# Performance work log

Measured on AMD Instinct MI355X. Metric: run time of the kernel, lower is better.

Reference implementation:

```python
import jax, jax.numpy as jnp
import numpy as np

# Mamba2 hyperparams (from config['block'][0])
D_MODEL = 512
D_STATE = 64
D_CONV = 4
EXPAND = 2
HEADDIM = 64
D_INNER = EXPAND * D_MODEL          # 1024
NHEADS = D_INNER // HEADDIM         # 16
CONV_DIM = D_INNER + 2 * D_STATE    # 1152 (x, B, C share the depthwise conv)
D_IN_PROJ = 2 * D_INNER + 2 * D_STATE + NHEADS  # z | xBC | dt
EPS = 1e-5
BATCH, SEQLEN = 2, 4096


def setup_inputs() -> dict:
    key = jax.random.key(0)
    ks = jax.random.split(key, 10)
    x = jax.random.normal(ks[0], (BATCH, SEQLEN, D_MODEL), dtype=jnp.float32)
    W_in = jax.random.normal(ks[1], (D_MODEL, D_IN_PROJ), dtype=jnp.float32) * 0.02
    conv_w = jax.random.normal(ks[2], (CONV_DIM, 1, D_CONV), dtype=jnp.float32) * 0.2
    conv_b = jax.random.normal(ks[3], (CONV_DIM,), dtype=jnp.float32) * 0.02
    dt_bias = jax.random.uniform(ks[4], (NHEADS,), minval=-4.0, maxval=-1.0, dtype=jnp.float32)
    A_log = jnp.log(jax.random.uniform(ks[5], (NHEADS,), minval=1.0, maxval=16.0, dtype=jnp.float32))
    D = jax.random.normal(ks[6], (NHEADS,), dtype=jnp.float32) * 0.5 + 1.0
    norm_weight = jnp.ones((D_INNER,), dtype=jnp.float32)
    W_out = jax.random.normal(ks[7], (D_INNER, D_MODEL), dtype=jnp.float32) * 0.02
    return {"x": x, "W_in": W_in, "conv_w": conv_w, "conv_b": conv_b,
            "dt_bias": dt_bias, "A_log": A_log, "D": D,
            "norm_weight": norm_weight, "W_out": W_out}


def _mamba2_forward(x, W_in, conv_w, conv_b, dt_bias, A_log, D, norm_weight, W_out):
    b, l, _ = x.shape
    zxbcdt = x @ W_in                                      # (b, l, D_IN_PROJ)
    z = zxbcdt[..., :D_INNER]                              # gate branch
    xBC = zxbcdt[..., D_INNER:D_INNER + CONV_DIM]
    dt = zxbcdt[..., D_INNER + CONV_DIM:]                  # (b, l, h)

    # depthwise causal conv1d over sequence, then SiLU
    xBC_ncw = jnp.transpose(xBC, (0, 2, 1))                # (b, c, l)
    xBC_ncw = jax.lax.conv_general_dilated(
        xBC_ncw, conv_w, window_strides=(1,), padding=[(D_CONV - 1, 0)],
        dimension_numbers=("NCW", "OIW", "NCW"), feature_group_count=CONV_DIM)
    xBC_ncw = xBC_ncw + conv_b[None, :, None]
    xBC = jax.nn.silu(jnp.transpose(xBC_ncw, (0, 2, 1)))   # (b, l, c)

    x_ssm = xBC[..., :D_INNER].reshape(b, l, NHEADS, HEADDIM)  # (b,l,h,p)
    B = xBC[..., D_INNER:D_INNER + D_STATE]                    # (b,l,n)
    C = xBC[..., D_INNER + D_STATE:]                           # (b,l,n)

    dt = jax.nn.softplus(dt + dt_bias)                     # (b,l,h)
    A = -jnp.exp(A_log)                                    # (h,)
    dA = jnp.exp(dt * A)                                   # (b,l,h) discrete decay

    # selective scan: state s has shape (b, h, p, n)
    def step(s, inp):
        dA_t, dt_t, x_t, B_t, C_t = inp                    # (b,h),(b,h),(b,h,p),(b,n),(b,n)
        dBx = (dt_t[..., None] * x_t)[..., None] * B_t[:, None, None, :]
        s = s * dA_t[..., None, None] + dBx
        y_t = jnp.einsum("bhpn,bn->bhp", s, C_t)
        return s, y_t

    s0 = jnp.zeros((b, NHEADS, HEADDIM, D_STATE), dtype=x.dtype)
    xs = (jnp.moveaxis(dA, 1, 0), jnp.moveaxis(dt, 1, 0),
          jnp.moveaxis(x_ssm, 1, 0), jnp.moveaxis(B, 1, 0), jnp.moveaxis(C, 1, 0))
    _, ys = jax.lax.scan(step, s0, xs)                     # ys: (l,b,h,p)
    y = jnp.moveaxis(ys, 0, 1)                             # (b,l,h,p)

    y = y + D[None, None, :, None] * x_ssm                 # skip term
    y = y.reshape(b, l, D_INNER)

    # gated RMSNorm (norm after gating, mamba2 default)
    y = y * jax.nn.silu(z)
    var = jnp.mean(jnp.square(y), axis=-1, keepdims=True)
    y = y * jax.lax.rsqrt(var + EPS) * norm_weight

    return y @ W_out                                       # (b, l, d_model)


def reference(x, W_in, conv_w, conv_b, dt_bias, A_log, D, norm_weight, W_out):
    return _mamba2_forward(x, W_in, conv_w, conv_b, dt_bias, A_log, D, norm_weight, W_out)
```

## Files before the change

kernel.cpp:

```cpp
#include <hip/hip_runtime.h>
#include <hip/hip_bf16.h>

#define BATCH   2
#define SEQ     4096
#define DMODEL  512
#define DINNER  1024
#define DSTATE  64
#define NHEADS  16
#define HEADDIM 64
#define CONVDIM 1152
#define NPROJ   2192
#define NPROJ_PAD 2304
#define MROWS   (BATCH*SEQ)
#define QCH     64
#define NCHUNK  (SEQ/QCH)

typedef short bf16x8 __attribute__((ext_vector_type(8)));
typedef float f32x4  __attribute__((ext_vector_type(4)));
using bf16 = __hip_bfloat16;
typedef unsigned short ushort_t;
typedef unsigned int   uint_t;

__device__ __forceinline__ float sigmoidf_(float x) { return 1.f / (1.f + __expf(-x)); }
__device__ __forceinline__ float bf2f(ushort_t u) { return __uint_as_float((uint_t)u << 16); }
__device__ __forceinline__ ushort_t f2bfu(float f) {
    bf16 h = __float2bfloat16(f);
    return *(ushort_t*)&h;
}
__device__ __forceinline__ void bf8_to_f(const ushort_t* __restrict__ p, float* __restrict__ f) {
    uint4 u = *(const uint4*)p;
    f[0] = __uint_as_float((u.x & 0xFFFFu) << 16);
    f[1] = __uint_as_float(u.x & 0xFFFF0000u);
    f[2] = __uint_as_float((u.y & 0xFFFFu) << 16);
    f[3] = __uint_as_float(u.y & 0xFFFF0000u);
    f[4] = __uint_as_float((u.z & 0xFFFFu) << 16);
    f[5] = __uint_as_float(u.z & 0xFFFF0000u);
    f[6] = __uint_as_float((u.w & 0xFFFFu) << 16);
    f[7] = __uint_as_float(u.w & 0xFFFF0000u);
}
__device__ __forceinline__ uint4 f8_to_bf(const float* __restrict__ f) {
    union { ushort_t s[8]; uint4 u; } r;
#pragma unroll
    for (int i = 0; i < 8; i++) r.s[i] = f2bfu(f[i]);
    return r.u;
}

__device__ __forceinline__ void gload_lds16(const ushort_t* g, ushort_t* l)
{
    __builtin_amdgcn_global_load_lds(
        (const __attribute__((address_space(1))) void*)g,
        (__attribute__((address_space(3)))       void*)l,
        16, 0, 0);
}

__global__ void cast_f32_bf16_k(const float* __restrict__ in, ushort_t* __restrict__ out, int n8)
{
    int i = blockIdx.x * 256 + threadIdx.x;
    if (i >= n8) return;
    float f[8];
    *(float4*)(f + 0) = ((const float4*)in)[i * 2 + 0];
    *(float4*)(f + 4) = ((const float4*)in)[i * 2 + 1];
    ((uint4*)out)[i] = f8_to_bf(f);
}

__global__ void transpose_f32_bf16_k(const float* __restrict__ in, ushort_t* __restrict__ out,
                                     int R, int C, int Cpad, const float* __restrict__ sv)
{
    __shared__ __align__(16) ushort_t tile[32][33];
    int c0 = blockIdx.x * 32, r0 = blockIdx.y * 32;
    int tx = threadIdx.x, ty = threadIdx.y;
#pragma unroll
    for (int i = 0; i < 32; i += 8) {
        int r = r0 + ty + i, c = c0 + tx;
        float v = (r < R && c < C) ? in[(size_t)r * C + c] : 0.f;
        if (sv && r < R) v *= sv[r];
        tile[ty + i][tx] = f2bfu(v);
    }
    __syncthreads();
#pragma unroll
    for (int i = 0; i < 32; i += 8) {
        int orow = c0 + ty + i, ocol = r0 + tx;
        if (orow < Cpad && ocol < R) out[(size_t)orow * R + ocol] = tile[tx][ty + i];
    }
}

__global__ void bcconv_k(const ushort_t* __restrict__ xpbc, const float* __restrict__ cw,
                         const float* __restrict__ cb, ushort_t* __restrict__ bcc)
{
    int idx = blockIdx.x * 256 + threadIdx.x;
    int row = idx >> 4, c8 = (idx & 15) * 8;
    int l = row & (SEQ - 1);
    float acc[8];
#pragma unroll
    for (int i = 0; i < 8; i++) acc[i] = cb[1024 + c8 + i];
#pragma unroll
    for (int j = 0; j < 4; j++) {
        int ll = l - 3 + j;
        if (ll >= 0) {
            float v[8];
            bf8_to_f(xpbc + (size_t)(row - 3 + j) * 128 + c8, v);
#pragma unroll
            for (int i = 0; i < 8; i++) acc[i] += cw[(1024 + c8 + i) * 4 + j] * v[i];
        }
    }
#pragma unroll
    for (int i = 0; i < 8; i++) { float v = acc[i]; acc[i] = v * sigmoidf_(v); }
    *(uint4*)(bcc + (size_t)row * 128 + c8) = f8_to_bf(acc);
}

__global__ __launch_bounds__(256, 4)
void xconv_k(const ushort_t* __restrict__ xpre, const float* __restrict__ cw,
             const float* __restrict__ cb, ushort_t* __restrict__ xs)
{
    const int c8 = (threadIdx.x & 127) * 8;
    const int rh = threadIdx.x >> 7;
    const int b  = blockIdx.y;
    const int l0 = blockIdx.x * 32 + rh * 16;
    float w[4][8], cbv[8];
#pragma unroll
    for (int i = 0; i < 8; i++) {
        cbv[i] = cb[c8 + i];
        float4 wv = *(const float4*)(cw + (size_t)(c8 + i) * 4);
        w[0][i] = wv.x; w[1][i] = wv.y; w[2][i] = wv.z; w[3][i] = wv.w;
    }
    float win[3][8];
#pragma unroll
    for (int j = 0; j < 3; j++) {
        int ll = l0 - 3 + j;
        if (ll >= 0) bf8_to_f(xpre + ((size_t)b * SEQ + ll) * 1024 + c8, win[j]);
        else {
#pragma unroll
            for (int i = 0; i < 8; i++) win[j][i] = 0.f;
        }
    }
#pragma unroll 4
    for (int r = 0; r < 16; r++) {
        int l = l0 + r;
        float cur[8], o[8];
        bf8_to_f(xpre + ((size_t)b * SEQ + l) * 1024 + c8, cur);
#pragma unroll
        for (int i = 0; i < 8; i++) {
            float a = cbv[i] + w[0][i] * win[0][i] + w[1][i] * win[1][i]
                             + w[2][i] * win[2][i] + w[3][i] * cur[i];
            o[i] = a * sigmoidf_(a);
        }
        *(uint4*)(xs + ((size_t)b * SEQ + l) * 1024 + c8) = f8_to_bf(o);
#pragma unroll
        for (int i = 0; i < 8; i++) { win[0][i] = win[1][i]; win[1][i] = win[2][i]; win[2][i] = cur[i]; }
    }
}

template<int MODE>
__global__ __launch_bounds__(256, MODE == 1 ? 4 : 3)
void gemm_k(const ushort_t* __restrict__ A, const ushort_t* __restrict__ Bt,
            ushort_t* __restrict__ zbuf, ushort_t* __restrict__ xpx,
            ushort_t* __restrict__ xpbc, float* __restrict__ dtv,
            float* __restrict__ dalog, const float* __restrict__ dt_b,
            const float* __restrict__ A_log, float* __restrict__ outf,
            int M, int N, int K)
{
    constexpr int TN = (MODE == 1) ? 64 : 128;
    constexpr int NJ = TN / 32;
    constexpr int SC = 132;
    constexpr int SMEM_ELTS = (MODE == 1) ? (128 * 64 + TN * 64) : (128 * SC);
    __shared__ __align__(16) ushort_t smem[SMEM_ELTS];
    ushort_t* As = smem;
    ushort_t* Bs = smem + 128 * 64;
    ushort_t* Cs = smem;

    const int tid  = threadIdx.x;
    const int wave = tid >> 6, lane = tid & 63;
    const int quad = lane >> 4, l16 = lane & 15;
    const int wm = (wave >> 1) * 64, wn = (wave & 1) * (TN / 2);

    const int GX = gridDim.x;
    int lin = blockIdx.y * GX + blockIdx.x;
    const int cpx = (GX * gridDim.y) >> 3;
    lin = (lin & 7) * cpx + (lin >> 3);
    const int m0 = (lin / GX) * 128, n0 = (lin % GX) * TN;

    const int srow = lane >> 3;
    const int scol = (lane & 7) * 8;
    const ushort_t* ag = A  + (size_t)(m0 + wave * 32       + srow) * K + scol;
    const ushort_t* bg = Bt + (size_t)(n0 + wave * (TN / 4) + srow) * K + scol;
    ushort_t* al = As + wave * 32 * 64;
    ushort_t* bl = Bs + wave * (TN / 4) * 64;

    f32x4 acc[4][NJ];
#pragma unroll
    for (int i = 0; i < 4; i++)
#pragma unroll
        for (int j = 0; j < NJ; j++) acc[i][j] = (f32x4){0.f, 0.f, 0.f, 0.f};
    float ssq4[4] = {0.f, 0.f, 0.f, 0.f};

    for (int k0 = 0; k0 < K; k0 += 64) {
        __syncthreads();
#pragma unroll
        for (int j = 0; j < 4; j++)
            gload_lds16(ag + (size_t)(j * 8) * K + k0, al + j * 8 * 64);
#pragma unroll
        for (int j = 0; j < NJ; j++)
            gload_lds16(bg + (size_t)(j * 8) * K + k0, bl + j * 8 * 64);
        __syncthreads();
#pragma unroll
        for (int kk = 0; kk < 64; kk += 32) {
            bf16x8 af[4], bfr[NJ];
#pragma unroll
            for (int i = 0; i < 4; i++)
                af[i] = *(const bf16x8*)(&As[(wm + i * 16 + l16) * 64 + kk + quad * 8]);
#pragma unroll
            for (int j = 0; j < NJ; j++)
                bfr[j] = *(const bf16x8*)(&Bs[(wn + j * 16 + l16) * 64 + kk + quad * 8]);
#pragma unroll
            for (int i = 0; i < 4; i++)
#pragma unroll
                for (int j = 0; j < NJ; j++)
                    acc[i][j] = __builtin_amdgcn_mfma_f32_16x16x32_bf16(af[i], bfr[j], acc[i][j], 0, 0, 0);
            if (MODE == 1 && (wave & 1) == 0) {
#pragma unroll
                for (int i = 0; i < 4; i++)
#pragma unroll
                    for (int e = 0; e < 8; e++) {
                        float f = bf2f((ushort_t)af[i][e]);
                        ssq4[i] += f * f;
                    }
            }
        }
    }
    if (MODE == 1) {
        __syncthreads();
        float* smemf = (float*)smem;
        if ((wave & 1) == 0) {
#pragma unroll
            for (int i = 0; i < 4; i++) {
                float s = ssq4[i];
                s += __shfl_xor(s, 16, 64);
                s += __shfl_xor(s, 32, 64);
                if (quad == 0) smemf[wm + i * 16 + l16] = s;
            }
        }
        __syncthreads();
#pragma unroll
        for (int i = 0; i < 4; i++)
#pragma unroll
            for (int j = 0; j < NJ; j++) {
                int col  = n0 + wn + j * 16 + l16;
                int rowl = wm + i * 16 + quad * 4;
#pragma unroll
                for (int r = 0; r < 4; r++) {
                    float sc = rsqrtf(smemf[rowl + r] * (1.f / DINNER) + 1e-5f);
                    outf[(size_t)(m0 + rowl + r) * N + col] = acc[i][j][r] * sc;
                }
            }
    } else if (n0 == 2176) {
#pragma unroll
        for (int i = 0; i < 4; i++)
#pragma unroll
            for (int j = 0; j < NJ; j++) {
                int col = n0 + wn + j * 16 + l16;
                int rowb = m0 + wm + i * 16 + quad * 4;
                if (col < N) {
                    int hh = col - 2176;
#pragma unroll
                    for (int r = 0; r < 4; r++) {
                        float v = acc[i][j][r];
                        size_t g = (size_t)hh * MROWS + (rowb + r);
                        float raw = v + dt_b[hh];
                        float sp  = (raw > 20.f) ? raw : log1pf(__expf(raw));
                        dtv  [g] = sp;
                        dalog[g] = -__expf(A_log[hh]) * sp;
                    }
                }
            }
    } else {
        __syncthreads();
#pragma unroll
        for (int i = 0; i < 4; i++)
#pragma unroll
            for (int j = 0; j < NJ; j++)
#pragma unroll
                for (int r = 0; r < 4; r++)
                    Cs[(wm + i * 16 + quad * 4 + r) * SC + wn + j * 16 + l16] = f2bfu(acc[i][j][r]);
        __syncthreads();
        ushort_t* dst; int ld, coff;
        if (n0 < 1024)      { dst = zbuf; ld = 1024; coff = n0; }
        else if (n0 < 2048) { dst = xpx;  ld = 1024; coff = n0 - 1024; }
        else                { dst = xpbc; ld = 128;  coff = 0; }
#pragma unroll
        for (int jj = 0; jj < 8; jj++) {
            int idx = jj * 256 + tid;
            int row = idx >> 4, cq = (idx & 15) * 8;
            uint4 v = *(const uint4*)&Cs[row * SC + cq];
            *(uint4*)&dst[(size_t)(m0 + row) * ld + coff + cq] = v;
        }
    }
}

__global__ __launch_bounds__(256, 3)
void chunk_state_k(const ushort_t* __restrict__ xs, const ushort_t* __restrict__ bcc,
                   const float* __restrict__ dtv, const float* __restrict__ dalog,
                   ushort_t* __restrict__ statesT, float* __restrict__ cdecay)
{
    const int c = blockIdx.x, h = blockIdx.y, b = blockIdx.z;
    __shared__ __align__(16) ushort_t xsT[64 * 72];
    __shared__ __align__(16) ushort_t BwT[64 * 72];
    __shared__ float wc[64];
    const int tid = threadIdx.x;
    const int ts = tid >> 2, q4 = (tid & 3) * 16;
    const int l = c * QCH + ts;
    if (tid < 64) {
        size_t gl = (size_t)h * MROWS + (size_t)b * SEQ + c * QCH + tid;
        float v = dalog[gl];
#pragma unroll
        for (int off = 1; off < 64; off <<= 1) {
            float u = __shfl_up(v, off, 64);
            if (tid >= off) v += u;
        }
        float tot = __shfl(v, 63, 64);
        wc[tid] = __expf(tot - v) * dtv[gl];
        if (tid == 63) cdecay[(c * BATCH + b) * NHEADS + h] = __expf(tot);
    }
    {
        const int ch0 = h * HEADDIM + q4;
        const ushort_t* rp = xs + ((size_t)b * SEQ + l) * 1024 + ch0;
        union { uint4 u; ushort_t s[8]; } u0, u1;
        u0.u = *(const uint4*)rp; u1.u = *(const uint4*)(rp + 8);
#pragma unroll
        for (int i = 0; i < 8; i++) {
            xsT[(q4 + i) * 72 + ts]     = u0.s[i];
            xsT[(q4 + 8 + i) * 72 + ts] = u1.s[i];
        }
    }
    __syncthreads();
    {
        float bv[16];
        const ushort_t* rp = bcc + ((size_t)b * SEQ + l) * 128;
        bf8_to_f(rp + q4, bv); bf8_to_f(rp + q4 + 8, bv + 8);
        const float wt = wc[ts];
#pragma unroll
        for (int i = 0; i < 16; i++) BwT[(q4 + i) * 72 + ts] = f2bfu(bv[i] * wt);
    }
    __syncthreads();
    const int wave = tid >> 6, lane = tid & 63;
    const int quad = lane >> 4, l16 = lane & 15;
    f32x4 acc[4];
#pragma unroll
    for (int j = 0; j < 4; j++) acc[j] = (f32x4){0.f, 0.f, 0.f, 0.f};
#pragma unroll
    for (int kk = 0; kk < 64; kk += 32) {
        bf16x8 af = *(const bf16x8*)(&xsT[(wave * 16 + l16) * 72 + kk + quad * 8]);
#pragma unroll
        for (int j = 0; j < 4; j++) {
            bf16x8 bf_ = *(const bf16x8*)(&BwT[(j * 16 + l16) * 72 + kk + quad * 8]);
            acc[j] = __builtin_amdgcn_mfma_f32_16x16x32_bf16(af, bf_, acc[j], 0, 0, 0);
        }
    }
    ushort_t* base = statesT + ((size_t)(c * BATCH + b) * NHEADS + h) * (HEADDIM * DSTATE);
#pragma unroll
    for (int j = 0; j < 4; j++)
#pragma unroll
        for (int r = 0; r < 4; r++)
            base[(wave * 16 + quad * 4 + r) * 64 + j * 16 + l16] = f2bfu(acc[j][r]);
}

__global__ void scan_combine_k(ushort_t* __restrict__ states, const float* __restrict__ cdecay)
{
    const int blk = blockIdx.x;
    const int eighth = blk & 7;
    const int h = (blk >> 3) & 15;
    const int b = blk >> 7;
    const int tid = threadIdx.x;
    __shared__ float dec[64];
    if (tid < 64) dec[tid] = cdecay[(tid * BATCH + b) * NHEADS + h];
    __syncthreads();
    const size_t cstride = (size_t)BATCH * NHEADS * HEADDIM * DSTATE;
    ushort_t* base = states + ((size_t)b * NHEADS + h) * (HEADDIM * DSTATE) + eighth * 512 + tid * 4;
    float sx = 0.f, sy = 0.f, sz = 0.f, sw = 0.f;
    uint2 pre[4];
#pragma unroll
    for (int j = 0; j < 4; j++) pre[j] = *(const uint2*)(base + j * cstride);
    for (int c = 0; c < NCHUNK; c++) {
        uint2 Sc = pre[c & 3];
        if (c + 4 < NCHUNK) pre[c & 3] = *(const uint2*)(base + (size_t)(c + 4) * cstride);
        float d = dec[c];
        uint2 o;
        o.x = (uint_t)f2bfu(sx) | ((uint_t)f2bfu(sy) << 16);
        o.y = (uint_t)f2bfu(sz) | ((uint_t)f2bfu(sw) << 16);
        *(uint2*)(base + (size_t)c * cstride) = o;
        sx = d * sx + __uint_as_float((Sc.x & 0xFFFFu) << 16);
        sy = d * sy + __uint_as_float(Sc.x & 0xFFFF0000u);
        sz = d * sz + __uint_as_float((Sc.y & 0xFFFFu) << 16);
        sw = d * sw + __uint_as_float(Sc.y & 0xFFFF0000u);
    }
}

__global__ __launch_bounds__(256, 3)
void chunk_y_k(const ushort_t* __restrict__ xs, const ushort_t* __restrict__ bcc,
               ushort_t* zio,
               const float* __restrict__ dtv, const float* __restrict__ dalog,
               const ushort_t* __restrict__ statesT, const float* __restrict__ Dp)
{
    const int c = blockIdx.x, h = blockIdx.y, b = blockIdx.z;
    __shared__ __align__(16) ushort_t CLb [64 * 72];
    __shared__ __align__(16) ushort_t BLb [64 * 72];
    __shared__ __align__(16) ushort_t xsT [64 * 72];
    __shared__ __align__(16) ushort_t attL[64 * 72];
    __shared__ float cum[64], wdt[64];
    const int tid = threadIdx.x;
    const int ts = tid >> 2, q4 = (tid & 3) * 16;
    const int l = c * QCH + ts;
    const float Dh = Dp[h];
    {
        const int ch0 = h * HEADDIM + q4;
        const ushort_t* rp = xs + ((size_t)b * SEQ + l) * 1024 + ch0;
        union { uint4 u; ushort_t s[8]; } u0, u1;
        u0.u = *(const uint4*)rp; u1.u = *(const uint4*)(rp + 8);
#pragma unroll
        for (int i = 0; i < 8; i++) {
            xsT[(q4 + i) * 72 + ts]     = u0.s[i];
            xsT[(q4 + 8 + i) * 72 + ts] = u1.s[i];
        }
    }
    {
        const ushort_t* rp = bcc + ((size_t)b * SEQ + l) * 128;
        *(uint4*)&BLb[ts * 72 + q4]     = *(const uint4*)(rp + q4);
        *(uint4*)&BLb[ts * 72 + q4 + 8] = *(const uint4*)(rp + q4 + 8);
        *(uint4*)&CLb[ts * 72 + q4]     = *(const uint4*)(rp + 64 + q4);
        *(uint4*)&CLb[ts * 72 + q4 + 8] = *(const uint4*)(rp + 64 + q4 + 8);
    }
    if (tid < 64) {
        size_t gl = (size_t)h * MROWS + (size_t)b * SEQ + c * QCH + tid;
        float v = dalog[gl];
#pragma unroll
        for (int off = 1; off < 64; off <<= 1) {
            float u = __shfl_up(v, off, 64);
            if (tid >= off) v += u;
        }
        cum[tid] = v;
        wdt[tid] = dtv[gl];
    }
    __syncthreads();
    const int wave = tid >> 6, lane = tid & 63;
    const int quad = lane >> 4, l16 = lane & 15;
    {
        f32x4 sacc[4];
#pragma unroll
        for (int j = 0; j < 4; j++) sacc[j] = (f32x4){0.f, 0.f, 0.f, 0.f};
#pragma unroll
        for (int kk = 0; kk < 64; kk += 32) {
            bf16x8 af = *(const bf16x8*)(&CLb[(wave * 16 + l16) * 72 + kk + quad * 8]);
#pragma unroll
            for (int j = 0; j < 4; j++) {
                bf16x8 bf_ = *(const bf16x8*)(&BLb[(j * 16 + l16) * 72 + kk + quad * 8]);
                sacc[j] = __builtin_amdgcn_mfma_f32_16x16x32_bf16(af, bf_, sacc[j], 0, 0, 0);
            }
        }
#pragma unroll
        for (int r = 0; r < 4; r++) {
            const int t = wave * 16 + quad * 4 + r;
            const float ct = cum[t];
#pragma unroll
            for (int j = 0; j < 4; j++) {
                const int s = j * 16 + l16;
                float a = (s <= t) ? sacc[j][r] * __expf(ct - cum[s]) * wdt[s] : 0.f;
                attL[t * 72 + s] = f2bfu(a);
            }
        }
    }
    __syncthreads();
    {
        f32x4 accY[4], accI[4];
#pragma unroll
        for (int j = 0; j < 4; j++) { accY[j] = (f32x4){0.f, 0.f, 0.f, 0.f}; accI[j] = (f32x4){0.f, 0.f, 0.f, 0.f}; }
        const ushort_t* spg = statesT + ((size_t)(c * BATCH + b) * NHEADS + h) * (HEADDIM * DSTATE);
#pragma unroll
        for (int kk = 0; kk < 64; kk += 32) {
            bf16x8 a2 = *(const bf16x8*)(&attL[(wave * 16 + l16) * 72 + kk + quad * 8]);
            bf16x8 a3 = *(const bf16x8*)(&CLb [(wave * 16 + l16) * 72 + kk + quad * 8]);
#pragma unroll
            for (int j = 0; j < 4; j++) {
                bf16x8 b2 = *(const bf16x8*)(&xsT[(j * 16 + l16) * 72 + kk + quad * 8]);
                accY[j] = __builtin_amdgcn_mfma_f32_16x16x32_bf16(a2, b2, accY[j], 0, 0, 0);
                bf16x8 b3 = *(const bf16x8*)(spg + (j * 16 + l16) * 64 + kk + quad * 8);
                accI[j] = __builtin_amdgcn_mfma_f32_16x16x32_bf16(a3, b3, accI[j], 0, 0, 0);
            }
        }
#pragma unroll
        for (int r = 0; r < 4; r++) {
            const int t = wave * 16 + quad * 4 + r;
            const float et = __expf(cum[t]);
#pragma unroll
            for (int j = 0; j < 4; j++) {
                const int p = j * 16 + l16;
                float xv = bf2f(xsT[p * 72 + t]);
                float y = accY[j][r] + et * accI[j][r] + Dh * xv;
                BLb[t * 72 + p] = f2bfu(y);
            }
        }
    }
    __syncthreads();
    {
        ushort_t* zrow = zio + ((size_t)b * SEQ + l) * DINNER + h * HEADDIM + q4;
        float zv[16], yv[16], o[16];
        bf8_to_f(zrow, zv); bf8_to_f(zrow + 8, zv + 8);
        bf8_to_f(&BLb[ts * 72 + q4], yv); bf8_to_f(&BLb[ts * 72 + q4 + 8], yv + 8);
#pragma unroll
        for (int j = 0; j < 16; j++) {
            float z = zv[j];
            o[j] = yv[j] * z * sigmoidf_(z);
        }
        *(uint4*)(zrow)     = f8_to_bf(o);
        *(uint4*)(zrow + 8) = f8_to_bf(o + 8);
    }
}

extern "C" void kernel_launch(void* const* d_in, const int* in_sizes, int n_in,
                              void* d_out, int out_size, void* d_ws, size_t ws_size,
                              hipStream_t stream)
{
    const float* x      = (const float*)d_in[0];
    const float* W_in   = (const float*)d_in[1];
    const float* conv_w = (const float*)d_in[2];
    const float* conv_b = (const float*)d_in[3];
    const float* dt_b   = (const float*)d_in[4];
    const float* A_log  = (const float*)d_in[5];
    const float* Dp     = (const float*)d_in[6];
    const float* nw     = (const float*)d_in[7];
    const float* W_out  = (const float*)d_in[8];
    float* out = (float*)d_out;

    char* w = (char*)d_ws;
    ushort_t* zbuf    = (ushort_t*)(w);
    ushort_t* xs      = (ushort_t*)(w + 16777216);
    ushort_t* xpre    = (ushort_t*)(w + 33554432);
    ushort_t* statesT = (ushort_t*)(w + 33554432);
    ushort_t* WoutT   = (ushort_t*)(w + 33554432);
    char* dscr = (char*)d_out;
    ushort_t* xpbc  = (ushort_t*)(dscr);
    float*    dtv   = (float*)(dscr + 2097152);
    float*    dalog = (float*)(dscr + 2621440);
    float*    cdec  = (float*)(dscr + 3145728);
    ushort_t* WinT  = (ushort_t*)(dscr + 4194304);
    ushort_t* bcc   = (ushort_t*)(dscr + 4194304);
    ushort_t* xb    = (ushort_t*)(dscr + 8388608);

    cast_f32_bf16_k<<<(MROWS * DMODEL / 8 + 255) / 256, 256, 0, stream>>>(x, xb, MROWS * DMODEL / 8);
    transpose_f32_bf16_k<<<dim3(NPROJ_PAD / 32, DMODEL / 32), dim3(32, 8), 0, stream>>>(W_in, WinT, DMODEL, NPROJ, NPROJ_PAD, nullptr);
    gemm_k<0><<<dim3(NPROJ_PAD / 128, MROWS / 128), 256, 0, stream>>>(
        xb, WinT, zbuf, xpre, xpbc, dtv, dalog, dt_b, A_log, nullptr,
        MROWS, NPROJ, DMODEL);
    bcconv_k<<<MROWS * 16 / 256, 256, 0, stream>>>(xpbc, conv_w, conv_b, bcc);
    xconv_k<<<dim3(SEQ / 32, BATCH), 256, 0, stream>>>(xpre, conv_w, conv_b, xs);
    chunk_state_k<<<dim3(NCHUNK, NHEADS, BATCH), 256, 0, stream>>>(
        xs, bcc, dtv, dalog, statesT, cdec);
    scan_combine_k<<<BATCH * NHEADS * 8, 128, 0, stream>>>(statesT, cdec);
    chunk_y_k<<<dim3(NCHUNK, NHEADS, BATCH), 256, 0, stream>>>(
        xs, bcc, zbuf, dtv, dalog, statesT, Dp);
    transpose_f32_bf16_k<<<dim3(DMODEL / 32, DINNER / 32), dim3(32, 8), 0, stream>>>(W_out, WoutT, DINNER, DMODEL, DMODEL, nw);
    gemm_k<1><<<dim3(DMODEL / 64, MROWS / 128), 256, 0, stream>>>(
        zbuf, WoutT, nullptr, nullptr, nullptr, nullptr, nullptr, nullptr,
        nullptr, out, MROWS, DMODEL, DINNER);
}
```

Baseline: 221.6 us.

## Merge prep and conv launches; XOR-swizzle transposed LDS tiles in chunk kernels

Combines the x cast and both weight transposes into one prep kernel, and the B/C conv and x conv into one conv kernel. This cuts the launch count by three. WoutT is moved into the output scratch region so it can be built at the start instead of after chunk_y. The transposed xsT/BwT stores and reads in chunk_state and chunk_y now use an XOR swizzle on the column index to reduce LDS bank conflicts during the column-wise writes. The swizzle must match on every read site; a missed index would corrupt results.

```diff
diff --git a/kernel.cpp b/kernel.cpp
--- a/kernel.cpp
+++ b/kernel.cpp
@@ -53,22 +53,35 @@
         16, 0, 0);
 }
 
-__global__ void cast_f32_bf16_k(const float* __restrict__ in, ushort_t* __restrict__ out, int n8)
-{
-    int i = blockIdx.x * 256 + threadIdx.x;
-    if (i >= n8) return;
-    float f[8];
-    *(float4*)(f + 0) = ((const float4*)in)[i * 2 + 0];
-    *(float4*)(f + 4) = ((const float4*)in)[i * 2 + 1];
-    ((uint4*)out)[i] = f8_to_bf(f);
-}
-
-__global__ void transpose_f32_bf16_k(const float* __restrict__ in, ushort_t* __restrict__ out,
-                                     int R, int C, int Cpad, const float* __restrict__ sv)
+__global__ __launch_bounds__(256, 4)
+void prep_k(const float* __restrict__ x, ushort_t* __restrict__ xb,
+            const float* __restrict__ W_in, ushort_t* __restrict__ WinT,
+            const float* __restrict__ W_out, ushort_t* __restrict__ WoutT,
+            const float* __restrict__ nw)
 {
     __shared__ __align__(16) ushort_t tile[32][33];
-    int c0 = blockIdx.x * 32, r0 = blockIdx.y * 32;
-    int tx = threadIdx.x, ty = threadIdx.y;
+    const int bid = blockIdx.x, tid = threadIdx.x;
+    if (bid < 2048) {
+        int i = bid * 256 + tid;
+        float f[8];
+        *(float4*)(f + 0) = ((const float4*)x)[i * 2 + 0];
+        *(float4*)(f + 4) = ((const float4*)x)[i * 2 + 1];
+        ((uint4*)xb)[i] = f8_to_bf(f);
+        return;
+    }
+    const int tx = tid & 31, ty = tid >> 5;
+    const float* in; ushort_t* out; int R, C, Cpad; const float* sv;
+    int bx, by;
+    if (bid < 3200) {
+        int b2 = bid - 2048;
+        bx = b2 % (NPROJ_PAD / 32); by = b2 / (NPROJ_PAD / 32);
+        in = W_in; out = WinT; R = DMODEL; C = NPROJ; Cpad = NPROJ_PAD; sv = nullptr;
+    } else {
+        int b3 = bid - 3200;
+        bx = b3 % (DMODEL / 32); by = b3 / (DMODEL / 32);
+        in = W_out; out = WoutT; R = DINNER; C = DMODEL; Cpad = DMODEL; sv = nw;
+    }
+    int c0 = bx * 32, r0 = by * 32;
 #pragma unroll
     for (int i = 0; i < 32; i += 8) {
         int r = r0 + ty + i, c = c0 + tx;
@@ -84,38 +97,39 @@
     }
 }
 
-__global__ void bcconv_k(const ushort_t* __restrict__ xpbc, const float* __restrict__ cw,
-                         const float* __restrict__ cb, ushort_t* __restrict__ bcc)
-{
-    int idx = blockIdx.x * 256 + threadIdx.x;
-    int row = idx >> 4, c8 = (idx & 15) * 8;
-    int l = row & (SEQ - 1);
-    float acc[8];
-#pragma unroll
-    for (int i = 0; i < 8; i++) acc[i] = cb[1024 + c8 + i];
-#pragma unroll
-    for (int j = 0; j < 4; j++) {
-        int ll = l - 3 + j;
-        if (ll >= 0) {
-            float v[8];
-            bf8_to_f(xpbc + (size_t)(row - 3 + j) * 128 + c8, v);
-#pragma unroll
-            for (int i = 0; i < 8; i++) acc[i] += cw[(1024 + c8 + i) * 4 + j] * v[i];
-        }
-    }
-#pragma unroll
-    for (int i = 0; i < 8; i++) { float v = acc[i]; acc[i] = v * sigmoidf_(v); }
-    *(uint4*)(bcc + (size_t)row * 128 + c8) = f8_to_bf(acc);
-}
-
 __global__ __launch_bounds__(256, 4)
-void xconv_k(const ushort_t* __restrict__ xpre, const float* __restrict__ cw,
-             const float* __restrict__ cb, ushort_t* __restrict__ xs)
-{
-    const int c8 = (threadIdx.x & 127) * 8;
-    const int rh = threadIdx.x >> 7;
-    const int b  = blockIdx.y;
-    const int l0 = blockIdx.x * 32 + rh * 16;
+void conv_k(const ushort_t* __restrict__ xpbc, const ushort_t* __restrict__ xpre,
+            const float* __restrict__ cw, const float* __restrict__ cb,
+            ushort_t* __restrict__ bcc, ushort_t* __restrict__ xs)
+{
+    const int bid = blockIdx.x, tid = threadIdx.x;
+    if (bid < 512) {
+        int idx = bid * 256 + tid;
+        int row = idx >> 4, c8 = (idx & 15) * 8;
+        int l = row & (SEQ - 1);
+        float acc[8];
+#pragma unroll
+        for (int i = 0; i < 8; i++) acc[i] = cb[1024 + c8 + i];
+#pragma unroll
+        for (int j = 0; j < 4; j++) {
+            int ll = l - 3 + j;
+            if (ll >= 0) {
+                float v[8];
+                bf8_to_f(xpbc + (size_t)(row - 3 + j) * 128 + c8, v);
+#pragma unroll
+                for (int i = 0; i < 8; i++) acc[i] += cw[(1024 + c8 + i) * 4 + j] * v[i];
+            }
+        }
+#pragma unroll
+        for (int i = 0; i < 8; i++) { float v = acc[i]; acc[i] = v * sigmoidf_(v); }
+        *(uint4*)(bcc + (size_t)row * 128 + c8) = f8_to_bf(acc);
+        return;
+    }
+    const int b2 = bid - 512;
+    const int gx = b2 & 127, b = b2 >> 7;
+    const int c8 = (tid & 127) * 8;
+    const int rh = tid >> 7;
+    const int l0 = gx * 32 + rh * 16;
     float w[4][8], cbv[8];
 #pragma unroll
     for (int i = 0; i < 8; i++) {
@@ -308,6 +322,7 @@
     const int tid = threadIdx.x;
     const int ts = tid >> 2, q4 = (tid & 3) * 16;
     const int l = c * QCH + ts;
+    const int tswz = ts ^ ((tid & 3) << 3);
     if (tid < 64) {
         size_t gl = (size_t)h * MROWS + (size_t)b * SEQ + c * QCH + tid;
         float v = dalog[gl];
@@ -327,8 +342,8 @@
         u0.u = *(const uint4*)rp; u1.u = *(const uint4*)(rp + 8);
 #pragma unroll
         for (int i = 0; i < 8; i++) {
-            xsT[(q4 + i) * 72 + ts]     = u0.s[i];
-            xsT[(q4 + 8 + i) * 72 + ts] = u1.s[i];
+            xsT[(q4 + i) * 72 + tswz]     = u0.s[i];
+            xsT[(q4 + 8 + i) * 72 + tswz] = u1.s[i];
         }
     }
     __syncthreads();
@@ -338,7 +353,7 @@
         bf8_to_f(rp + q4, bv); bf8_to_f(rp + q4 + 8, bv + 8);
         const float wt = wc[ts];
 #pragma unroll
-        for (int i = 0; i < 16; i++) BwT[(q4 + i) * 72 + ts] = f2bfu(bv[i] * wt);
+        for (int i = 0; i < 16; i++) BwT[(q4 + i) * 72 + tswz] = f2bfu(bv[i] * wt);
     }
     __syncthreads();
     const int wave = tid >> 6, lane = tid & 63;
@@ -348,10 +363,10 @@
     for (int j = 0; j < 4; j++) acc[j] = (f32x4){0.f, 0.f, 0.f, 0.f};
 #pragma unroll
     for (int kk = 0; kk < 64; kk += 32) {
-        bf16x8 af = *(const bf16x8*)(&xsT[(wave * 16 + l16) * 72 + kk + quad * 8]);
+        bf16x8 af = *(const bf16x8*)(&xsT[(wave * 16 + l16) * 72 + ((kk + quad * 8) ^ ((wave & 3) << 3))]);
 #pragma unroll
         for (int j = 0; j < 4; j++) {
-            bf16x8 bf_ = *(const bf16x8*)(&BwT[(j * 16 + l16) * 72 + kk + quad * 8]);
+            bf16x8 bf_ = *(const bf16x8*)(&BwT[(j * 16 + l16) * 72 + ((kk + quad * 8) ^ ((j & 3) << 3))]);
             acc[j] = __builtin_amdgcn_mfma_f32_16x16x32_bf16(af, bf_, acc[j], 0, 0, 0);
         }
     }
@@ -409,6 +424,7 @@
     const int tid = threadIdx.x;
     const int ts = tid >> 2, q4 = (tid & 3) * 16;
     const int l = c * QCH + ts;
+    const int tswz = ts ^ ((tid & 3) << 3);
     const float Dh = Dp[h];
     {
         const int ch0 = h * HEADDIM + q4;
@@ -417,8 +433,8 @@
         u0.u = *(const uint4*)rp; u1.u = *(const uint4*)(rp + 8);
 #pragma unroll
         for (int i = 0; i < 8; i++) {
-            xsT[(q4 + i) * 72 + ts]     = u0.s[i];
-            xsT[(q4 + 8 + i) * 72 + ts] = u1.s[i];
+            xsT[(q4 + i) * 72 + tswz]     = u0.s[i];
+            xsT[(q4 + 8 + i) * 72 + tswz] = u1.s[i];
         }
     }
     {
@@ -479,7 +495,7 @@
             bf16x8 a3 = *(const bf16x8*)(&CLb [(wave * 16 + l16) * 72 + kk + quad * 8]);
 #pragma unroll
             for (int j = 0; j < 4; j++) {
-                bf16x8 b2 = *(const bf16x8*)(&xsT[(j * 16 + l16) * 72 + kk + quad * 8]);
+                bf16x8 b2 = *(const bf16x8*)(&xsT[(j * 16 + l16) * 72 + ((kk + quad * 8) ^ ((j & 3) << 3))]);
                 accY[j] = __builtin_amdgcn_mfma_f32_16x16x32_bf16(a2, b2, accY[j], 0, 0, 0);
                 bf16x8 b3 = *(const bf16x8*)(spg + (j * 16 + l16) * 64 + kk + quad * 8);
                 accI[j] = __builtin_amdgcn_mfma_f32_16x16x32_bf16(a3, b3, accI[j], 0, 0, 0);
@@ -492,7 +508,7 @@
 #pragma unroll
             for (int j = 0; j < 4; j++) {
                 const int p = j * 16 + l16;
-                float xv = bf2f(xsT[p * 72 + t]);
+                float xv = bf2f(xsT[p * 72 + (t ^ ((j & 3) << 3))]);
                 float y = accY[j][r] + et * accI[j][r] + Dh * xv;
                 BLb[t * 72 + p] = f2bfu(y);
             }
@@ -534,7 +550,6 @@
     ushort_t* xs      = (ushort_t*)(w + 16777216);
     ushort_t* xpre    = (ushort_t*)(w + 33554432);
     ushort_t* statesT = (ushort_t*)(w + 33554432);
-    ushort_t* WoutT   = (ushort_t*)(w + 33554432);
     char* dscr = (char*)d_out;
     ushort_t* xpbc  = (ushort_t*)(dscr);
     float*    dtv   = (float*)(dscr + 2097152);
@@ -542,21 +557,20 @@
     float*    cdec  = (float*)(dscr + 3145728);
     ushort_t* WinT  = (ushort_t*)(dscr + 4194304);
     ushort_t* bcc   = (ushort_t*)(dscr + 4194304);
+    ushort_t* WoutT = (ushort_t*)(dscr + 6815744);
     ushort_t* xb    = (ushort_t*)(dscr + 8388608);
 
-    cast_f32_bf16_k<<<(MROWS * DMODEL / 8 + 255) / 256, 256, 0, stream>>>(x, xb, MROWS * DMODEL / 8);
-    transpose_f32_bf16_k<<<dim3(NPROJ_PAD / 32, DMODEL / 32), dim3(32, 8), 0, stream>>>(W_in, WinT, DMODEL, NPROJ, NPROJ_PAD, nullptr);
+    prep_k<<<2048 + (NPROJ_PAD / 32) * (DMODEL / 32) + (DMODEL / 32) * (DINNER / 32), 256, 0, stream>>>(
+        x, xb, W_in, WinT, W_out, WoutT, nw);
     gemm_k<0><<<dim3(NPROJ_PAD / 128, MROWS / 128), 256, 0, stream>>>(
         xb, WinT, zbuf, xpre, xpbc, dtv, dalog, dt_b, A_log, nullptr,
         MROWS, NPROJ, DMODEL);
-    bcconv_k<<<MROWS * 16 / 256, 256, 0, stream>>>(xpbc, conv_w, conv_b, bcc);
-    xconv_k<<<dim3(SEQ / 32, BATCH), 256, 0, stream>>>(xpre, conv_w, conv_b, xs);
+    conv_k<<<512 + 256, 256, 0, stream>>>(xpbc, xpre, conv_w, conv_b, bcc, xs);
     chunk_state_k<<<dim3(NCHUNK, NHEADS, BATCH), 256, 0, stream>>>(
         xs, bcc, dtv, dalog, statesT, cdec);
     scan_combine_k<<<BATCH * NHEADS * 8, 128, 0, stream>>>(statesT, cdec);
     chunk_y_k<<<dim3(NCHUNK, NHEADS, BATCH), 256, 0, stream>>>(
         xs, bcc, zbuf, dtv, dalog, statesT, Dp);
-    transpose_f32_bf16_k<<<dim3(DMODEL / 32, DINNER / 32), dim3(32, 8), 0, stream>>>(W_out, WoutT, DINNER, DMODEL, DMODEL, nw);
     gemm_k<1><<<dim3(DMODEL / 64, MROWS / 128), 256, 0, stream>>>(
         zbuf, WoutT, nullptr, nullptr, nullptr, nullptr, nullptr, nullptr,
         nullptr, out, MROWS, DMODEL, DINNER);
```

Result: faster. 205.4 us (-7.3%).
